# Performance work log

Hardware: AMD Instinct MI355X
Metric: run time of the kernel (lower is better)

Reference implementation:

```python
import jax, jax.numpy as jnp
import numpy as np

DIM = 1024
NUM_HEADS = 16
HEAD_DIM = DIM // NUM_HEADS


def setup_inputs() -> dict:
    key = jax.random.key(0)
    k1, k2, k3 = jax.random.split(key, 3)
    B, T = 2, 2048
    x = jax.random.normal(k1, (B, T, DIM), dtype=jnp.float32)
    w_qkv = jax.random.normal(k2, (DIM, 3 * DIM), dtype=jnp.float32) * (DIM ** -0.5)
    b_qkv = jnp.zeros((3 * DIM,), dtype=jnp.float32)
    w_proj = jax.random.normal(k3, (DIM, DIM), dtype=jnp.float32) * (DIM ** -0.5)
    b_proj = jnp.zeros((DIM,), dtype=jnp.float32)
    return {"x": x, "w_qkv": w_qkv, "b_qkv": b_qkv, "w_proj": w_proj, "b_proj": b_proj}


def reference(x, w_qkv, b_qkv, w_proj, b_proj):
    B, T, C = x.shape
    H, D = NUM_HEADS, HEAD_DIM
    scale = jnp.asarray(D ** -0.5, dtype=x.dtype)
    # qkv projection -> (B, T, 3, H, D)
    qkv = (x @ w_qkv + b_qkv).reshape(B, T, 3, H, D)
    q = qkv[:, :, 0].transpose(0, 2, 1, 3)  # (B, H, T, D)
    k = qkv[:, :, 1].transpose(0, 2, 1, 3)
    v = qkv[:, :, 2].transpose(0, 2, 1, 3)
    q = q * scale
    # scores (B, H, T, T), softmax in fp32 as in the original
    attn = jnp.einsum('bhqd,bhkd->bhqk', q, k)
    attn = jax.nn.softmax(attn.astype(jnp.float32), axis=-1).astype(v.dtype)
    out = jnp.einsum('bhqk,bhkd->bhqd', attn, v)  # (B, H, T, D)
    out = out.transpose(0, 2, 1, 3).reshape(B, T, C)
    return out @ w_proj + b_proj
```

## Files before the change

### kernel.cpp

```cpp
#include <hip/hip_runtime.h>

typedef __attribute__((ext_vector_type(8))) short short8;
typedef __attribute__((ext_vector_type(4))) float f32x4;

#define DIM_C 1024
#define NHEAD 16
#define HDIM  64
#define BB    2
#define TT    2048
#define NELEM ((size_t)BB * NHEAD * TT * HDIM)

__device__ __forceinline__ short f2b(float f) {
    union { float f; unsigned u; } c; c.f = f;
    unsigned r = c.u + 0x7FFFu + ((c.u >> 16) & 1u);
    return (short)(r >> 16);
}
__device__ __forceinline__ float b2f(short s) {
    union { unsigned u; float f; } c; c.u = ((unsigned)(unsigned short)s) << 16;
    return c.f;
}
__device__ __forceinline__ void gload_lds16(const short* g, short* l) {
    __builtin_amdgcn_global_load_lds(
        (const __attribute__((address_space(1))) unsigned int*)g,
        (__attribute__((address_space(3))) unsigned int*)l, 16, 0, 0);
}

__global__ __launch_bounds__(256) void split_f32(const float* __restrict__ X,
                                                 short* __restrict__ H,
                                                 short* __restrict__ L, int n4)
{
    const int i = blockIdx.x * 256 + threadIdx.x;
    if (i >= n4) return;
    float4 v = ((const float4*)X)[i];
    short h0 = f2b(v.x), h1 = f2b(v.y), h2 = f2b(v.z), h3 = f2b(v.w);
    short l0 = f2b(v.x - b2f(h0)), l1 = f2b(v.y - b2f(h1));
    short l2 = f2b(v.z - b2f(h2)), l3 = f2b(v.w - b2f(h3));
    typedef __attribute__((ext_vector_type(4))) short short4v;
    ((short4v*)H)[i] = (short4v){h0, h1, h2, h3};
    ((short4v*)L)[i] = (short4v){l0, l1, l2, l3};
}

__global__ __launch_bounds__(256) void transpose_split(const float* __restrict__ W,
                                                       short* __restrict__ Th,
                                                       short* __restrict__ Tl,
                                                       int K, int N)
{
    __shared__ float T[32][33];
    const int tx = threadIdx.x & 31, ty = threadIdx.x >> 5;
    const int n0 = blockIdx.x * 32, k0 = blockIdx.y * 32;
#pragma unroll
    for (int i = 0; i < 4; ++i)
        T[ty + i * 8][tx] = W[(size_t)(k0 + ty + i * 8) * N + n0 + tx];
    __syncthreads();
#pragma unroll
    for (int i = 0; i < 4; ++i) {
        const int n = ty + i * 8;
        const float v = T[tx][n];
        const short hi = f2b(v);
        Th[(size_t)(n0 + n) * K + k0 + tx] = hi;
        Tl[(size_t)(n0 + n) * K + k0 + tx] = f2b(v - b2f(hi));
    }
}

template <int EPI>
__global__ __launch_bounds__(256) void gemm_mfma(
    const short* __restrict__ Ah, const short* __restrict__ Al,
    const short* __restrict__ BTh, const short* __restrict__ BTl,
    const float* __restrict__ bias,
    float* __restrict__ outF,
    short* __restrict__ qh_, short* __restrict__ ql_,
    short* __restrict__ kh_, short* __restrict__ kl_,
    short* __restrict__ vh_, short* __restrict__ vl_,
    int M, int N, int K)
{
    __shared__ short As_h[128 * 64];
    __shared__ short As_l[128 * 64];
    __shared__ short Bs_h[128 * 64];
    __shared__ short Bs_l[128 * 64];

    const int tid  = threadIdx.x;
    const int lane = tid & 63;
    const int wid  = tid >> 6;
    const int wr   = wid >> 1, wc = wid & 1;
    const int g    = lane >> 4, lr = lane & 15;
    const int row0 = blockIdx.y * 128;
    const int col0 = blockIdx.x * 128;

    f32x4 acc[4][4];
#pragma unroll
    for (int m = 0; m < 4; ++m)
#pragma unroll
        for (int n = 0; n < 4; ++n) acc[m][n] = (f32x4){0.f, 0.f, 0.f, 0.f};

    for (int k0 = 0; k0 < K; k0 += 64) {
        __syncthreads();
#pragma unroll
        for (int c = 0; c < 4; ++c) {
            const int idx = c * 256 + tid;
            const int r   = idx >> 3;
            const int ss  = (idx & 7) ^ (r & 7);
            const size_t srcA = (size_t)(row0 + r) * K + k0 + ss * 8;
            const size_t srcB = (size_t)(col0 + r) * K + k0 + ss * 8;
            gload_lds16(Ah + srcA, &As_h[idx * 8]);
            gload_lds16(Al + srcA, &As_l[idx * 8]);
            gload_lds16(BTh + srcB, &Bs_h[idx * 8]);
            gload_lds16(BTl + srcB, &Bs_l[idx * 8]);
        }
        __syncthreads();

        short8 bhf[4][2], blf[4][2];
#pragma unroll
        for (int n = 0; n < 4; ++n)
#pragma unroll
            for (int ks = 0; ks < 2; ++ks) {
                const int r    = wc * 64 + n * 16 + lr;
                const int slot = (ks * 4 + g) ^ (r & 7);
                bhf[n][ks] = *(const short8*)&Bs_h[r * 64 + slot * 8];
                blf[n][ks] = *(const short8*)&Bs_l[r * 64 + slot * 8];
            }
#pragma unroll
        for (int m = 0; m < 4; ++m) {
            short8 ahf[2], alf[2];
#pragma unroll
            for (int ks = 0; ks < 2; ++ks) {
                const int r    = wr * 64 + m * 16 + lr;
                const int slot = (ks * 4 + g) ^ (r & 7);
                ahf[ks] = *(const short8*)&As_h[r * 64 + slot * 8];
                alf[ks] = *(const short8*)&As_l[r * 64 + slot * 8];
            }
#pragma unroll
            for (int n = 0; n < 4; ++n)
#pragma unroll
                for (int ks = 0; ks < 2; ++ks) {
                    acc[m][n] = __builtin_amdgcn_mfma_f32_16x16x32_bf16(ahf[ks], bhf[n][ks], acc[m][n], 0, 0, 0);
                    acc[m][n] = __builtin_amdgcn_mfma_f32_16x16x32_bf16(alf[ks], bhf[n][ks], acc[m][n], 0, 0, 0);
                    acc[m][n] = __builtin_amdgcn_mfma_f32_16x16x32_bf16(ahf[ks], blf[n][ks], acc[m][n], 0, 0, 0);
                }
        }
    }

#pragma unroll
    for (int m = 0; m < 4; ++m) {
#pragma unroll
        for (int n = 0; n < 4; ++n) {
#pragma unroll
            for (int r = 0; r < 4; ++r) {
                const int grow = row0 + wr * 64 + m * 16 + g * 4 + r;
                const int gcol = col0 + wc * 64 + n * 16 + lr;
                const float vv = acc[m][n][r] + bias[gcol];
                if (EPI == 0) {
                    const int b     = grow / TT;
                    const int t     = grow % TT;
                    const int which = gcol >> 10;
                    const int rem   = gcol & 1023;
                    const int h     = rem >> 6;
                    const int d     = rem & 63;
                    if (which == 0) {
                        const size_t idx = (((size_t)(b * NHEAD + h)) * TT + t) * HDIM + d;
                        const float sv = vv * 0.125f;
                        const short hi = f2b(sv);
                        qh_[idx] = hi; ql_[idx] = f2b(sv - b2f(hi));
                    } else if (which == 1) {
                        const size_t idx = (((size_t)(b * NHEAD + h)) * TT + t) * HDIM + d;
                        const short hi = f2b(vv);
                        kh_[idx] = hi; kl_[idx] = f2b(vv - b2f(hi));
                    } else {
                        const int t32 = t & 31;
                        const int u = t32 >> 4, gq = (t32 >> 2) & 3, rr = t32 & 3;
                        const int tp = (t & ~31) | (gq * 8 + u * 4 + rr);
                        const size_t idx = ((size_t)((b * NHEAD + h) * HDIM + d)) * TT + tp;
                        const short hi = f2b(vv);
                        vh_[idx] = hi; vl_[idx] = f2b(vv - b2f(hi));
                    }
                } else {
                    outF[(size_t)grow * N + gcol] = vv;
                }
            }
        }
    }
}

__global__ __launch_bounds__(256, 2) void attn_mfma(
    const short* __restrict__ qh, const short* __restrict__ ql,
    const short* __restrict__ kh, const short* __restrict__ kl,
    const short* __restrict__ vth, const short* __restrict__ vtl,
    short* __restrict__ oh, short* __restrict__ ol)
{
    __shared__ short Kh_s[2][4096];
    __shared__ short Kl_s[2][4096];
    __shared__ short Vh_s[2][4096];
    __shared__ short Vl_s[2][4096];

    const int tid  = threadIdx.x;
    const int wid  = tid >> 6;
    const int lane = tid & 63;
    const int g    = lane >> 4;
    const int lr   = lane & 15;
    const int lr7  = lr & 7;

    const int bid = (blockIdx.x & 7) * (gridDim.x >> 3) + (blockIdx.x >> 3);
    const int bh  = bid >> 4;
    const int q0  = (bid & 15) * 128;
    const size_t base = (size_t)bh * TT * HDIM;

    short8 qhf[2][2], qlf[2][2];
#pragma unroll
    for (int qs = 0; qs < 2; ++qs) {
        const size_t qrow = base + (size_t)(q0 + wid * 32 + qs * 16 + lr) * HDIM;
#pragma unroll
        for (int ks = 0; ks < 2; ++ks) {
            qhf[qs][ks] = *(const short8*)(qh + qrow + ks * 32 + g * 8);
            qlf[qs][ks] = *(const short8*)(ql + qrow + ks * 32 + g * 8);
        }
    }

    f32x4 ofr[2][4];
#pragma unroll
    for (int qs = 0; qs < 2; ++qs)
#pragma unroll
        for (int dt = 0; dt < 4; ++dt) ofr[qs][dt] = (f32x4){0.f, 0.f, 0.f, 0.f};
    float lsum[2] = {0.f, 0.f};

    auto STAGE = [&](int bsel, int step) {
#pragma unroll
        for (int i = 0; i < 2; ++i) {
            const int c   = tid + i * 256;
            const int row = c >> 3;
            const int sl  = (c & 7) ^ (row & 7);
            const size_t srcK = base + (size_t)(step * 64 + row) * HDIM + sl * 8;
            const size_t srcV = ((size_t)(bh * HDIM + row)) * TT + step * 64 + sl * 8;
            gload_lds16(kh + srcK, &Kh_s[bsel][c * 8]);
            gload_lds16(kl + srcK, &Kl_s[bsel][c * 8]);
            gload_lds16(vth + srcV, &Vh_s[bsel][c * 8]);
            gload_lds16(vtl + srcV, &Vl_s[bsel][c * 8]);
        }
    };

    STAGE(0, 0);
    __syncthreads();

    for (int step = 0; step < TT / 64; ++step) {
        const int cur = step & 1;
        if (step + 1 < TT / 64) STAGE(cur ^ 1, step + 1);

        f32x4 sfr[4][2];
#pragma unroll
        for (int t = 0; t < 4; ++t)
#pragma unroll
            for (int qs = 0; qs < 2; ++qs) sfr[t][qs] = (f32x4){0.f, 0.f, 0.f, 0.f};
#pragma unroll
        for (int t = 0; t < 4; ++t) {
#pragma unroll
            for (int ks = 0; ks < 2; ++ks) {
                const int adr = (t * 16 + lr) * 64 + (((ks * 4 + g) ^ lr7) * 8);
                short8 k8h = *(const short8*)&Kh_s[cur][adr];
                short8 k8l = *(const short8*)&Kl_s[cur][adr];
#pragma unroll
                for (int qs = 0; qs < 2; ++qs) {
                    sfr[t][qs] = __builtin_amdgcn_mfma_f32_16x16x32_bf16(k8h, qhf[qs][ks], sfr[t][qs], 0, 0, 0);
                    sfr[t][qs] = __builtin_amdgcn_mfma_f32_16x16x32_bf16(k8l, qhf[qs][ks], sfr[t][qs], 0, 0, 0);
                    sfr[t][qs] = __builtin_amdgcn_mfma_f32_16x16x32_bf16(k8h, qlf[qs][ks], sfr[t][qs], 0, 0, 0);
                }
            }
        }

        short8 pah[2][2], pal[2][2];
#pragma unroll
        for (int qs = 0; qs < 2; ++qs)
#pragma unroll
            for (int ks = 0; ks < 2; ++ks)
#pragma unroll
                for (int t2 = 0; t2 < 2; ++t2) {
                    const int t = ks * 2 + t2;
#pragma unroll
                    for (int r = 0; r < 4; ++r) {
                        const float p = __expf(sfr[t][qs][r]);
                        lsum[qs] += p;
                        const short hi = f2b(p);
                        pah[qs][ks][t2 * 4 + r] = hi;
                        pal[qs][ks][t2 * 4 + r] = f2b(p - b2f(hi));
                    }
                }

#pragma unroll
        for (int dt = 0; dt < 4; ++dt) {
#pragma unroll
            for (int ks = 0; ks < 2; ++ks) {
                const int adr = (dt * 16 + lr) * 64 + (((ks * 4 + g) ^ lr7) * 8);
                short8 v8h = *(const short8*)&Vh_s[cur][adr];
                short8 v8l = *(const short8*)&Vl_s[cur][adr];
#pragma unroll
                for (int qs = 0; qs < 2; ++qs) {
                    ofr[qs][dt] = __builtin_amdgcn_mfma_f32_16x16x32_bf16(pah[qs][ks], v8h, ofr[qs][dt], 0, 0, 0);
                    ofr[qs][dt] = __builtin_amdgcn_mfma_f32_16x16x32_bf16(pal[qs][ks], v8h, ofr[qs][dt], 0, 0, 0);
                    ofr[qs][dt] = __builtin_amdgcn_mfma_f32_16x16x32_bf16(pah[qs][ks], v8l, ofr[qs][dt], 0, 0, 0);
                }
            }
        }
        __syncthreads();
    }

#pragma unroll
    for (int qs = 0; qs < 2; ++qs) {
        lsum[qs] += __shfl_xor(lsum[qs], 16, 64);
        lsum[qs] += __shfl_xor(lsum[qs], 32, 64);
    }
    float rl[2][4];
#pragma unroll
    for (int qs = 0; qs < 2; ++qs)
#pragma unroll
        for (int r = 0; r < 4; ++r)
            rl[qs][r] = 1.f / __shfl(lsum[qs], g * 4 + r, 64);

    const int b = bh >> 4, h = bh & 15;
#pragma unroll
    for (int qs = 0; qs < 2; ++qs)
#pragma unroll
        for (int r = 0; r < 4; ++r) {
            const int t = q0 + wid * 32 + qs * 16 + g * 4 + r;
#pragma unroll
            for (int dt = 0; dt < 4; ++dt) {
                const float v = ofr[qs][dt][r] * rl[qs][r];
                const short hi = f2b(v);
                const size_t off = ((size_t)b * TT + t) * DIM_C + h * HDIM + dt * 16 + lr;
                oh[off] = hi;
                ol[off] = f2b(v - b2f(hi));
            }
        }
}

extern "C" void kernel_launch(void* const* d_in, const int* in_sizes, int n_in,
                              void* d_out, int out_size, void* d_ws, size_t ws_size,
                              hipStream_t stream)
{
    const float* x      = (const float*)d_in[0];
    const float* w_qkv  = (const float*)d_in[1];
    const float* b_qkv  = (const float*)d_in[2];
    const float* w_proj = (const float*)d_in[3];
    const float* b_proj = (const float*)d_in[4];
    float* out = (float*)d_out;

    char* wsb = (char*)d_ws;
    const size_t MB = 1024 * 1024;
    short* xh_w = (short*)(wsb + 0 * MB);
    short* xl_w = (short*)(wsb + 8 * MB);
    short* oh_w = xh_w;
    short* ol_w = xl_w;
    short* wqTh = (short*)(wsb + 16 * MB);
    short* wqTl = (short*)(wsb + 22 * MB);
    short* wpTh = (short*)(wsb + 16 * MB);
    short* wpTl = (short*)(wsb + 18 * MB);
    short* qh_w = (short*)(wsb + 28 * MB);
    short* ql_w = (short*)(wsb + 36 * MB);
    short* kh_w = (short*)(wsb + 44 * MB);
    short* kl_w = (short*)(wsb + 52 * MB);
    short* vth_w = (short*)(wsb + 60 * MB);
    short* vtl_w = (short*)(wsb + 68 * MB);

    split_f32<<<dim3(NELEM / 4 / 256), 256, 0, stream>>>(x, xh_w, xl_w, NELEM / 4);
    transpose_split<<<dim3(3 * DIM_C / 32, DIM_C / 32), 256, 0, stream>>>(
        w_qkv, wqTh, wqTl, DIM_C, 3 * DIM_C);

    dim3 g1(3 * DIM_C / 128, BB * TT / 128);
    gemm_mfma<0><<<g1, 256, 0, stream>>>(xh_w, xl_w, wqTh, wqTl, b_qkv, nullptr,
                                         qh_w, ql_w, kh_w, kl_w, vth_w, vtl_w,
                                         BB * TT, 3 * DIM_C, DIM_C);

    transpose_split<<<dim3(DIM_C / 32, DIM_C / 32), 256, 0, stream>>>(
        w_proj, wpTh, wpTl, DIM_C, DIM_C);

    attn_mfma<<<dim3(512), 256, 0, stream>>>(
        qh_w, ql_w, kh_w, kl_w, vth_w, vtl_w, oh_w, ol_w);

    dim3 g2(DIM_C / 128, BB * TT / 128);
    gemm_mfma<1><<<g2, 256, 0, stream>>>(oh_w, ol_w, wpTh, wpTl, b_proj, out,
                                         nullptr, nullptr, nullptr, nullptr, nullptr, nullptr,
                                         BB * TT, DIM_C, DIM_C);
}
```

Measured before the change: 348.2 us.

## Double-buffer GEMM LDS tiles with 512-thread blocks and prefetched K stages

Restructures the split-bf16 MFMA GEMM to use 8 waves per block, a K tile of 32, and two LDS buffers. The next-next K slice is issued asynchronously while the current one is consumed, gated by vmcnt waits. MFMA sections get raised priority and explicit barriers. This is meant to hide global-to-LDS latency that the old load-sync-compute loop exposed, at the cost of more barriers per K step and a smaller per-wave tile.

After: 355.1 us. About the same (+2.0%).

```diff
diff --git a/kernel.cpp b/kernel.cpp
--- a/kernel.cpp
+++ b/kernel.cpp
@@ -63,7 +63,7 @@
 }
 
 template <int EPI>
-__global__ __launch_bounds__(256) void gemm_mfma(
+__global__ __launch_bounds__(512, 4) void gemm_mfma(
     const short* __restrict__ Ah, const short* __restrict__ Al,
     const short* __restrict__ BTh, const short* __restrict__ BTl,
     const float* __restrict__ bias,
@@ -73,80 +73,100 @@
     short* __restrict__ vh_, short* __restrict__ vl_,
     int M, int N, int K)
 {
-    __shared__ short As_h[128 * 64];
-    __shared__ short As_l[128 * 64];
-    __shared__ short Bs_h[128 * 64];
-    __shared__ short Bs_l[128 * 64];
+    __shared__ short As_h[2][128 * 32];
+    __shared__ short As_l[2][128 * 32];
+    __shared__ short Bs_h[2][128 * 32];
+    __shared__ short Bs_l[2][128 * 32];
 
     const int tid  = threadIdx.x;
     const int lane = tid & 63;
     const int wid  = tid >> 6;
-    const int wr   = wid >> 1, wc = wid & 1;
+    const int wr   = wid >> 2;
+    const int wc   = wid & 3;
     const int g    = lane >> 4, lr = lane & 15;
     const int row0 = blockIdx.y * 128;
     const int col0 = blockIdx.x * 128;
-
-    f32x4 acc[4][4];
+    const int KT   = K >> 5;
+
+    const int sr  = tid >> 2;
+    const int ss  = (tid & 3) ^ ((sr >> 1) & 3);
+    const size_t srcAb = (size_t)(row0 + sr) * K + ss * 8;
+    const size_t srcBb = (size_t)(col0 + sr) * K + ss * 8;
+
+    auto STAGE = [&](int kt, int b) {
+        const size_t ka = srcAb + kt * 32;
+        const size_t kb = srcBb + kt * 32;
+        gload_lds16(Ah + ka, &As_h[b][tid * 8]);
+        gload_lds16(Al + ka, &As_l[b][tid * 8]);
+        gload_lds16(BTh + kb, &Bs_h[b][tid * 8]);
+        gload_lds16(BTl + kb, &Bs_l[b][tid * 8]);
+    };
+
+    f32x4 acc[4][2];
 #pragma unroll
     for (int m = 0; m < 4; ++m)
 #pragma unroll
-        for (int n = 0; n < 4; ++n) acc[m][n] = (f32x4){0.f, 0.f, 0.f, 0.f};
-
-    for (int k0 = 0; k0 < K; k0 += 64) {
-        __syncthreads();
-#pragma unroll
-        for (int c = 0; c < 4; ++c) {
-            const int idx = c * 256 + tid;
-            const int r   = idx >> 3;
-            const int ss  = (idx & 7) ^ (r & 7);
-            const size_t srcA = (size_t)(row0 + r) * K + k0 + ss * 8;
-            const size_t srcB = (size_t)(col0 + r) * K + k0 + ss * 8;
-            gload_lds16(Ah + srcA, &As_h[idx * 8]);
-            gload_lds16(Al + srcA, &As_l[idx * 8]);
-            gload_lds16(BTh + srcB, &Bs_h[idx * 8]);
-            gload_lds16(BTl + srcB, &Bs_l[idx * 8]);
-        }
-        __syncthreads();
-
-        short8 bhf[4][2], blf[4][2];
-#pragma unroll
-        for (int n = 0; n < 4; ++n)
-#pragma unroll
-            for (int ks = 0; ks < 2; ++ks) {
-                const int r    = wc * 64 + n * 16 + lr;
-                const int slot = (ks * 4 + g) ^ (r & 7);
-                bhf[n][ks] = *(const short8*)&Bs_h[r * 64 + slot * 8];
-                blf[n][ks] = *(const short8*)&Bs_l[r * 64 + slot * 8];
-            }
-#pragma unroll
-        for (int m = 0; m < 4; ++m) {
+        for (int n = 0; n < 2; ++n) acc[m][n] = (f32x4){0.f, 0.f, 0.f, 0.f};
+
+    STAGE(0, 0);
+    STAGE(1, 1);
+
+    for (int t = 0; t < KT; ++t) {
+        const int c = t & 1;
+        if (t == KT - 1) { asm volatile("s_waitcnt vmcnt(0)" ::: "memory"); }
+        else             { asm volatile("s_waitcnt vmcnt(4)" ::: "memory"); }
+        __builtin_amdgcn_sched_barrier(0);
+        __builtin_amdgcn_s_barrier();
+        __builtin_amdgcn_sched_barrier(0);
+
+        short8 bhf[2], blf[2];
+#pragma unroll
+        for (int mh = 0; mh < 2; ++mh) {
+            if (mh == 0) {
+#pragma unroll
+                for (int n = 0; n < 2; ++n) {
+                    const int r  = wc * 32 + n * 16 + lr;
+                    const int sl = g ^ ((r >> 1) & 3);
+                    bhf[n] = *(const short8*)&Bs_h[c][r * 32 + sl * 8];
+                    blf[n] = *(const short8*)&Bs_l[c][r * 32 + sl * 8];
+                }
+            }
             short8 ahf[2], alf[2];
 #pragma unroll
-            for (int ks = 0; ks < 2; ++ks) {
-                const int r    = wr * 64 + m * 16 + lr;
-                const int slot = (ks * 4 + g) ^ (r & 7);
-                ahf[ks] = *(const short8*)&As_h[r * 64 + slot * 8];
-                alf[ks] = *(const short8*)&As_l[r * 64 + slot * 8];
-            }
-#pragma unroll
-            for (int n = 0; n < 4; ++n)
-#pragma unroll
-                for (int ks = 0; ks < 2; ++ks) {
-                    acc[m][n] = __builtin_amdgcn_mfma_f32_16x16x32_bf16(ahf[ks], bhf[n][ks], acc[m][n], 0, 0, 0);
-                    acc[m][n] = __builtin_amdgcn_mfma_f32_16x16x32_bf16(alf[ks], bhf[n][ks], acc[m][n], 0, 0, 0);
-                    acc[m][n] = __builtin_amdgcn_mfma_f32_16x16x32_bf16(ahf[ks], blf[n][ks], acc[m][n], 0, 0, 0);
-                }
-        }
+            for (int m2 = 0; m2 < 2; ++m2) {
+                const int r  = wr * 64 + (mh * 2 + m2) * 16 + lr;
+                const int sl = g ^ ((r >> 1) & 3);
+                ahf[m2] = *(const short8*)&As_h[c][r * 32 + sl * 8];
+                alf[m2] = *(const short8*)&As_l[c][r * 32 + sl * 8];
+            }
+            asm volatile("s_waitcnt lgkmcnt(0)" ::: "memory");
+            __builtin_amdgcn_sched_barrier(0);
+            __builtin_amdgcn_s_setprio(1);
+#pragma unroll
+            for (int m2 = 0; m2 < 2; ++m2)
+#pragma unroll
+                for (int n = 0; n < 2; ++n) {
+                    const int m = mh * 2 + m2;
+                    acc[m][n] = __builtin_amdgcn_mfma_f32_16x16x32_bf16(ahf[m2], bhf[n], acc[m][n], 0, 0, 0);
+                    acc[m][n] = __builtin_amdgcn_mfma_f32_16x16x32_bf16(alf[m2], bhf[n], acc[m][n], 0, 0, 0);
+                    acc[m][n] = __builtin_amdgcn_mfma_f32_16x16x32_bf16(ahf[m2], blf[n], acc[m][n], 0, 0, 0);
+                }
+            __builtin_amdgcn_s_setprio(0);
+            __builtin_amdgcn_sched_barrier(0);
+            __builtin_amdgcn_s_barrier();
+            __builtin_amdgcn_sched_barrier(0);
+        }
+        if (t + 2 < KT) STAGE(t + 2, c);
     }
 
 #pragma unroll
     for (int m = 0; m < 4; ++m) {
 #pragma unroll
-        for (int n = 0; n < 4; ++n) {
+        for (int n = 0; n < 2; ++n) {
 #pragma unroll
             for (int r = 0; r < 4; ++r) {
                 const int grow = row0 + wr * 64 + m * 16 + g * 4 + r;
-                const int gcol = col0 + wc * 64 + n * 16 + lr;
+                const int gcol = col0 + wc * 32 + n * 16 + lr;
                 const float vv = acc[m][n][r] + bias[gcol];
                 if (EPI == 0) {
                     const int b     = grow / TT;
@@ -362,7 +382,7 @@
         w_qkv, wqTh, wqTl, DIM_C, 3 * DIM_C);
 
     dim3 g1(3 * DIM_C / 128, BB * TT / 128);
-    gemm_mfma<0><<<g1, 256, 0, stream>>>(xh_w, xl_w, wqTh, wqTl, b_qkv, nullptr,
+    gemm_mfma<0><<<g1, 512, 0, stream>>>(xh_w, xl_w, wqTh, wqTl, b_qkv, nullptr,
                                          qh_w, ql_w, kh_w, kl_w, vth_w, vtl_w,
                                          BB * TT, 3 * DIM_C, DIM_C);
 
@@ -373,7 +393,7 @@
         qh_w, ql_w, kh_w, kl_w, vth_w, vtl_w, oh_w, ol_w);
 
     dim3 g2(DIM_C / 128, BB * TT / 128);
-    gemm_mfma<1><<<g2, 256, 0, stream>>>(oh_w, ol_w, wpTh, wpTl, b_proj, out,
+    gemm_mfma<1><<<g2, 512, 0, stream>>>(oh_w, ol_w, wpTh, wpTl, b_proj, out,
                                          nullptr, nullptr, nullptr, nullptr, nullptr, nullptr,
                                          BB * TT, DIM_C, DIM_C);
 }
```

## Double-buffer GEMM LDS tiles with interleaved prefetch and MFMA scheduling barriers

Applied to the files above, without the earlier changes.

Restructures the bf16-split GEMM main loop to use a BK=32 double-buffered LDS tile, prefetching the next K-slice via global_load_lds while MFMAs run on the current buffer. It precomputes swizzled LDS addresses, spreads the prefetch issue across sub-iterations, and adds sched_barrier/s_setprio/s_barrier fencing to control instruction interleaving. It also requests two blocks per CU through launch_bounds. The aim is to hide global load latency behind compute, at the cost of more barriers per K-step and a smaller K tile.

Result: no change. 347.4 us (-0.2%).

```diff
diff --git a/kernel.cpp b/kernel.cpp
--- a/kernel.cpp
+++ b/kernel.cpp
@@ -63,7 +63,7 @@
 }
 
 template <int EPI>
-__global__ __launch_bounds__(256) void gemm_mfma(
+__global__ __launch_bounds__(256, 2) void gemm_mfma(
     const short* __restrict__ Ah, const short* __restrict__ Al,
     const short* __restrict__ BTh, const short* __restrict__ BTl,
     const float* __restrict__ bias,
@@ -73,10 +73,10 @@
     short* __restrict__ vh_, short* __restrict__ vl_,
     int M, int N, int K)
 {
-    __shared__ short As_h[128 * 64];
-    __shared__ short As_l[128 * 64];
-    __shared__ short Bs_h[128 * 64];
-    __shared__ short Bs_l[128 * 64];
+    __shared__ short As_h[2][4096];
+    __shared__ short As_l[2][4096];
+    __shared__ short Bs_h[2][4096];
+    __shared__ short Bs_l[2][4096];
 
     const int tid  = threadIdx.x;
     const int lane = tid & 63;
@@ -85,6 +85,15 @@
     const int g    = lane >> 4, lr = lane & 15;
     const int row0 = blockIdx.y * 128;
     const int col0 = blockIdx.x * 128;
+    const int KT   = K >> 5;
+
+    const int c0 = tid, c1 = tid + 256;
+    const int r0 = c0 >> 2, ss0 = (c0 & 3) ^ (r0 & 3);
+    const int r1 = c1 >> 2, ss1 = (c1 & 3) ^ (r1 & 3);
+    const size_t srcA0 = (size_t)(row0 + r0) * K + ss0 * 8;
+    const size_t srcA1 = (size_t)(row0 + r1) * K + ss1 * 8;
+    const size_t srcB0 = (size_t)(col0 + r0) * K + ss0 * 8;
+    const size_t srcB1 = (size_t)(col0 + r1) * K + ss1 * 8;
 
     f32x4 acc[4][4];
 #pragma unroll
@@ -92,50 +101,81 @@
 #pragma unroll
         for (int n = 0; n < 4; ++n) acc[m][n] = (f32x4){0.f, 0.f, 0.f, 0.f};
 
-    for (int k0 = 0; k0 < K; k0 += 64) {
-        __syncthreads();
-#pragma unroll
-        for (int c = 0; c < 4; ++c) {
-            const int idx = c * 256 + tid;
-            const int r   = idx >> 3;
-            const int ss  = (idx & 7) ^ (r & 7);
-            const size_t srcA = (size_t)(row0 + r) * K + k0 + ss * 8;
-            const size_t srcB = (size_t)(col0 + r) * K + k0 + ss * 8;
-            gload_lds16(Ah + srcA, &As_h[idx * 8]);
-            gload_lds16(Al + srcA, &As_l[idx * 8]);
-            gload_lds16(BTh + srcB, &Bs_h[idx * 8]);
-            gload_lds16(BTl + srcB, &Bs_l[idx * 8]);
-        }
-        __syncthreads();
-
-        short8 bhf[4][2], blf[4][2];
-#pragma unroll
-        for (int n = 0; n < 4; ++n)
-#pragma unroll
-            for (int ks = 0; ks < 2; ++ks) {
-                const int r    = wc * 64 + n * 16 + lr;
-                const int slot = (ks * 4 + g) ^ (r & 7);
-                bhf[n][ks] = *(const short8*)&Bs_h[r * 64 + slot * 8];
-                blf[n][ks] = *(const short8*)&Bs_l[r * 64 + slot * 8];
-            }
-#pragma unroll
-        for (int m = 0; m < 4; ++m) {
-            short8 ahf[2], alf[2];
-#pragma unroll
-            for (int ks = 0; ks < 2; ++ks) {
-                const int r    = wr * 64 + m * 16 + lr;
-                const int slot = (ks * 4 + g) ^ (r & 7);
-                ahf[ks] = *(const short8*)&As_h[r * 64 + slot * 8];
-                alf[ks] = *(const short8*)&As_l[r * 64 + slot * 8];
-            }
-#pragma unroll
-            for (int n = 0; n < 4; ++n)
-#pragma unroll
-                for (int ks = 0; ks < 2; ++ks) {
-                    acc[m][n] = __builtin_amdgcn_mfma_f32_16x16x32_bf16(ahf[ks], bhf[n][ks], acc[m][n], 0, 0, 0);
-                    acc[m][n] = __builtin_amdgcn_mfma_f32_16x16x32_bf16(alf[ks], bhf[n][ks], acc[m][n], 0, 0, 0);
-                    acc[m][n] = __builtin_amdgcn_mfma_f32_16x16x32_bf16(ahf[ks], blf[n][ks], acc[m][n], 0, 0, 0);
+    int badr[4];
+#pragma unroll
+    for (int n = 0; n < 4; ++n) {
+        const int r = wc * 64 + n * 16 + lr;
+        badr[n] = (r * 4 + (g ^ (r & 3))) * 8;
+    }
+    int aadr[4];
+#pragma unroll
+    for (int p = 0; p < 4; ++p) {
+        const int r = wr * 64 + p * 16 + lr;
+        aadr[p] = (r * 4 + (g ^ (r & 3))) * 8;
+    }
+
+    gload_lds16(Ah  + srcA0, &As_h[0][c0 * 8]);
+    gload_lds16(Ah  + srcA1, &As_h[0][c1 * 8]);
+    gload_lds16(Al  + srcA0, &As_l[0][c0 * 8]);
+    gload_lds16(Al  + srcA1, &As_l[0][c1 * 8]);
+    gload_lds16(BTh + srcB0, &Bs_h[0][c0 * 8]);
+    gload_lds16(BTh + srcB1, &Bs_h[0][c1 * 8]);
+    gload_lds16(BTl + srcB0, &Bs_l[0][c0 * 8]);
+    gload_lds16(BTl + srcB1, &Bs_l[0][c1 * 8]);
+    asm volatile("s_waitcnt vmcnt(0)" ::: "memory");
+    __builtin_amdgcn_sched_barrier(0);
+    __builtin_amdgcn_s_barrier();
+    __builtin_amdgcn_sched_barrier(0);
+
+    for (int t = 0; t < KT; ++t) {
+        const int cur = t & 1;
+        const int kn  = (t + 1) * 32;
+        const bool more = (t + 1 < KT);
+        short8 bh[4], bl[4];
+
+#pragma unroll
+        for (int p = 0; p < 4; ++p) {
+            if (p == 0) {
+#pragma unroll
+                for (int n = 0; n < 4; ++n) {
+                    bh[n] = *(const short8*)&Bs_h[cur][badr[n]];
+                    bl[n] = *(const short8*)&Bs_l[cur][badr[n]];
                 }
+            }
+            short8 ah = *(const short8*)&As_h[cur][aadr[p]];
+            short8 al = *(const short8*)&As_l[cur][aadr[p]];
+
+            if (p == 0 && more) {
+                gload_lds16(Ah + srcA0 + kn, &As_h[cur ^ 1][c0 * 8]);
+                gload_lds16(Ah + srcA1 + kn, &As_h[cur ^ 1][c1 * 8]);
+                gload_lds16(Al + srcA0 + kn, &As_l[cur ^ 1][c0 * 8]);
+                gload_lds16(Al + srcA1 + kn, &As_l[cur ^ 1][c1 * 8]);
+            }
+            if (p == 1 && more) {
+                gload_lds16(BTh + srcB0 + kn, &Bs_h[cur ^ 1][c0 * 8]);
+                gload_lds16(BTh + srcB1 + kn, &Bs_h[cur ^ 1][c1 * 8]);
+                gload_lds16(BTl + srcB0 + kn, &Bs_l[cur ^ 1][c0 * 8]);
+                gload_lds16(BTl + srcB1 + kn, &Bs_l[cur ^ 1][c1 * 8]);
+            }
+
+            __builtin_amdgcn_s_barrier();
+            asm volatile("s_waitcnt lgkmcnt(0)" ::: "memory");
+            __builtin_amdgcn_sched_barrier(0);
+            __builtin_amdgcn_s_setprio(1);
+#pragma unroll
+            for (int n = 0; n < 4; ++n) {
+                acc[p][n] = __builtin_amdgcn_mfma_f32_16x16x32_bf16(ah, bh[n], acc[p][n], 0, 0, 0);
+                acc[p][n] = __builtin_amdgcn_mfma_f32_16x16x32_bf16(al, bh[n], acc[p][n], 0, 0, 0);
+                acc[p][n] = __builtin_amdgcn_mfma_f32_16x16x32_bf16(ah, bl[n], acc[p][n], 0, 0, 0);
+            }
+            __builtin_amdgcn_s_setprio(0);
+            __builtin_amdgcn_sched_barrier(0);
+            if (p == 3) {
+                asm volatile("s_waitcnt vmcnt(0)" ::: "memory");
+                __builtin_amdgcn_sched_barrier(0);
+            }
+            __builtin_amdgcn_s_barrier();
+            __builtin_amdgcn_sched_barrier(0);
         }
     }
 
```
